# Performance work log

Measured on AMD Instinct MI355X. Metric: run time of the kernel, lower is better.

The kernel has to match this reference:

```python
import jax, jax.numpy as jnp
import numpy as np

N_Q = 4  # qubits = input_size
H_GATE = jnp.array([[1.0, 1.0], [1.0, -1.0]], dtype=jnp.complex64) / np.sqrt(2.0)
# efficient-kan grid: grid_size=1, spline_order=3, range [-1,1], h=2
KAN_GRID = np.arange(-3, 5, dtype=np.float32) * 2.0 - 1.0  # [-7,-5,-3,-1,1,3,5,7]
SPLINE_ORDER = 3


def nqe_embed(x):
    # [B, n] -> [B, 2n-1]: append (pi - x_i)(pi - x_{i+1}) ZZ-feature-map terms
    return jnp.concatenate([x, (jnp.pi - x[:, :-1]) * (jnp.pi - x[:, 1:])], axis=1)


def apply_1q(state, U, q):
    # state [B,2,2,2,2]; single-qubit gate U [2,2] on qubit q
    state = jnp.moveaxis(state, q + 1, -1)
    state = state @ U.T
    return jnp.moveaxis(state, -1, q + 1)


def apply_rz_batched(state, theta, q):
    # RZ(theta_b) with per-batch angles; diagonal gate -> elementwise phase
    ph = jnp.exp(-0.5j * theta)  # [B]
    diag = jnp.stack([ph, jnp.conj(ph)], axis=-1)  # [B,2]
    shape = [state.shape[0], 1, 1, 1, 1]
    shape[q + 1] = 2
    return state * diag.reshape(shape)


def apply_cnot(state, c, t):
    s = jnp.moveaxis(state, (c + 1, t + 1), (-2, -1))
    s = jnp.stack([s[..., 0, :], s[..., 1, ::-1]], axis=-2)
    return jnp.moveaxis(s, (-2, -1), (c + 1, t + 1))


def feature_map(state, angles):
    # IQP-style embedding: H on all, RZ(a_q), then ZZ(a_{n+i}) on neighbors (2n-1 angles)
    for q in range(N_Q):
        state = apply_1q(state, H_GATE, q)
    for q in range(N_Q):
        state = apply_rz_batched(state, angles[:, q], q)
    for i in range(N_Q - 1):
        state = apply_cnot(state, i, i + 1)
        state = apply_rz_batched(state, angles[:, N_Q + i], i + 1)
        state = apply_cnot(state, i, i + 1)
    return state


def rot_mat(phi, theta, omega):
    # pennylane Rot = RZ(omega) RY(theta) RZ(phi)
    c = jnp.cos(theta / 2).astype(jnp.complex64)
    s = jnp.sin(theta / 2).astype(jnp.complex64)
    a = jnp.exp(-0.5j * (phi + omega)) * c
    b = -jnp.exp(0.5j * (phi - omega)) * s
    d = jnp.exp(-0.5j * (phi - omega)) * s
    e = jnp.exp(0.5j * (phi + omega)) * c
    return jnp.stack([jnp.stack([a, b]), jnp.stack([d, e])])


def ansatz(state, params):
    # StronglyEntanglingLayers: 2 layers x (Rot per qubit + CNOT ring), params [24]
    p = params.reshape(2, N_Q, 3)
    for l in range(2):
        for q in range(N_Q):
            state = apply_1q(state, rot_mat(p[l, q, 0], p[l, q, 1], p[l, q, 2]), q)
        for q in range(N_Q):
            state = apply_cnot(state, q, (q + 1) % N_Q)
    return state


def quantum_cell(hidden_ang, input_ang, p1, p2):
    # one QRNN step: embed hidden, ansatz1, embed input, ansatz2, measure <Z_q>
    B = hidden_ang.shape[0]
    state = jnp.zeros((B, 2, 2, 2, 2), jnp.complex64).at[:, 0, 0, 0, 0].set(1.0)
    state = ansatz(feature_map(state, hidden_ang), p1)
    state = ansatz(feature_map(state, input_ang), p2)
    probs = jnp.abs(state) ** 2  # [B,2,2,2,2]
    sign = jnp.array([1.0, -1.0], jnp.float32)
    evs = []
    for q in range(N_Q):
        shape = [1, 1, 1, 1, 1]
        shape[q + 1] = 2
        evs.append(jnp.sum(probs * sign.reshape(shape), axis=(1, 2, 3, 4)))
    return jnp.stack(evs, axis=1)  # [B,4]


def kan_forward(x, base_w, spline_w):
    # efficient-kan KANLinear: silu base path + B-spline path (grid_size=1, order=3)
    grid = jnp.asarray(KAN_GRID)
    xg = x[..., None]  # [B,in,1]
    bases = ((xg >= grid[:-1]) & (xg < grid[1:])).astype(x.dtype)  # [B,in,7]
    for k in range(1, SPLINE_ORDER + 1):
        bases = ((xg - grid[: -(k + 1)]) / (grid[k:-1] - grid[: -(k + 1)]) * bases[..., :-1]
                 + (grid[k + 1:] - xg) / (grid[k + 1:] - grid[1:-k]) * bases[..., 1:])
    B = x.shape[0]
    base = jax.nn.silu(x) @ base_w.T
    spline = bases.reshape(B, -1) @ spline_w.reshape(spline_w.shape[0], -1).T
    return base + spline  # [B, 2n-1]


def setup_inputs() -> dict:
    key = jax.random.key(0)
    ks = jax.random.split(key, 10)
    B, S, n = 16384, 256, 4
    return {
        "inputs": jax.random.uniform(ks[0], (B, S, n), jnp.float32),
        "initial_t": jax.random.uniform(ks[1], (B, 2 * n - 1), jnp.float32),
        "ansatz_params_1": jax.random.uniform(ks[2], (24,), jnp.float32),
        "ansatz_params_2": jax.random.uniform(ks[3], (24,), jnp.float32),
        "kan_base_w": jax.random.normal(ks[4], (2 * n - 1, n), jnp.float32) * 0.1,
        "kan_spline_w": jax.random.normal(ks[5], (2 * n - 1, n, 4), jnp.float32) * 0.1,
        "cls_w1": jax.random.normal(ks[6], (16, n), jnp.float32) * 0.3,
        "cls_b1": jnp.zeros((16,), jnp.float32),
        "cls_w2": jax.random.normal(ks[7], (1, 16), jnp.float32) * 0.2,
        "cls_b2": jnp.zeros((1,), jnp.float32),
    }


def reference(inputs, initial_t, ansatz_params_1, ansatz_params_2, kan_base_w,
              kan_spline_w, cls_w1, cls_b1, cls_w2, cls_b2):
    # inputs [B,S,n]
    x0 = nqe_embed(inputs[:, 0])
    hidden = quantum_cell(initial_t, x0, ansatz_params_1, ansatz_params_2)  # [B,4]

    @jax.checkpoint
    def step(hidden, x_t):
        h_ang = kan_forward(hidden, kan_base_w, kan_spline_w)  # [B,7]
        x_emb = nqe_embed(x_t)  # [B,7]
        hidden = quantum_cell(h_ang, x_emb, ansatz_params_1, ansatz_params_2)
        return hidden, None

    xs = jnp.swapaxes(inputs[:, 1:], 0, 1)  # [S-1,B,n]
    hidden, _ = jax.lax.scan(step, hidden, xs)
    h = jax.nn.relu(hidden @ cls_w1.T + cls_b1)
    return h @ cls_w2.T + cls_b2  # [B,1]
```

## Files before the change

kernel.cpp:

```cpp
#include <hip/hip_runtime.h>
#include <math.h>

#define DEV static __device__ __forceinline__

typedef float v2 __attribute__((ext_vector_type(2)));

template<int CTRL>
DEV float qperm(float x) {
    return __int_as_float(__builtin_amdgcn_mov_dpp(__float_as_int(x), CTRL, 0xF, 0xF, true));
}
DEV float lx1(float v)  { return qperm<0xB1>(v); }
DEV float lx2(float v)  { return qperm<0x4E>(v); }
DEV float x3f_(float v) { return qperm<0x1B>(v); }
DEV float ror8(float v) { return qperm<0x128>(v); }
DEV float rfl(float x)  { return __int_as_float(__builtin_amdgcn_readfirstlane(__float_as_int(x))); }

DEV v2 ror8v(v2 a){ return (v2){ror8(a.x), ror8(a.y)}; }
DEV v2 lx1v(v2 a) { return (v2){lx1(a.x), lx1(a.y)}; }
DEV v2 lx2v(v2 a) { return (v2){lx2(a.x), lx2(a.y)}; }
DEV v2 x3v(v2 a)  { return (v2){x3f_(a.x), x3f_(a.y)}; }
DEV v2 r8lx1v(v2 a){ return (v2){ror8(lx1(a.x)), ror8(lx1(a.y))}; }
DEV v2 r8lx2v(v2 a){ return (v2){ror8(lx2(a.x)), ror8(lx2(a.y))}; }

DEV v2 vswap(v2 a)  { return __builtin_shufflevector(a, a, 1, 0); }
DEV v2 vsplat(float f) { return (v2){f, f}; }
DEV v2 vfma(v2 a, v2 b, v2 c) { return __builtin_elementwise_fma(a, b, c); }

DEV v2 gup(v2 A, v2 P, float dr, v2 di, float orr, v2 oi) {
    v2 n = A * dr;
    n = vfma(vswap(A), di, n);
    n = vfma(P, vsplat(orr), n);
    n = vfma(vswap(P), oi, n);
    return n;
}

DEV void fsincos(float rev, float* s, float* c) {
    float f = __builtin_amdgcn_fractf(rev);
    *s = __builtin_amdgcn_sinf(f);
    *c = __builtin_amdgcn_cosf(f);
}

__global__ __launch_bounds__(256, 2)
void qrnn_kernel(const float* __restrict__ inputs, const float* __restrict__ initial_t,
                 const float* __restrict__ p1, const float* __restrict__ p2,
                 const float* __restrict__ kbw, const float* __restrict__ ksw,
                 const float* __restrict__ w1, const float* __restrict__ cb1,
                 const float* __restrict__ w2, const float* __restrict__ cb2,
                 float* __restrict__ out, int B, int S)
{
    const int tid    = blockIdx.x * blockDim.x + threadIdx.x;
    const int lane16 = threadIdx.x & 15;
    const int e      = (tid >> 4) * 2 + ((lane16 >> 2) & 1);
    if (e >= B) return;
    const int sub    = lane16 & 3;
    const bool b1    = ((lane16 >> 3) & 1) != 0;
    const bool b2 = (sub & 1) != 0, b3 = (sub & 2) != 0;
    const float z2f = b2 ? -1.f : 1.f;
    const float z3f = b3 ? -1.f : 1.f;
    const float z1f = b1 ? -1.f : 1.f;
    const float z12 = z1f * z2f, z23 = z2f * z3f, z13 = z1f * z3f;
    const float z123 = z1f * z23;
    const bool is0 = (sub == 0), is1 = (sub == 1), is2 = (sub == 2);

    const float REVC = -0.07957747154594767f;

    float u00r[4][4], u00i[4][4], u01r[4][4], u01i[4][4];
    const float* PP[2] = { p1, p2 };
#pragma unroll
    for (int aI = 0; aI < 2; ++aI) {
        const float* pp = PP[aI];
#pragma unroll
        for (int l = 0; l < 2; ++l) {
            const int idx = aI*2 + l;
#pragma unroll
            for (int q = 0; q < 4; ++q) {
                float phi = pp[l*12 + q*3 + 0];
                float tht = pp[l*12 + q*3 + 1];
                float omg = pp[l*12 + q*3 + 2];
                float st, ct; sincosf(0.5f*tht, &st, &ct);
                float sA, cA, sB, cB;
                sincosf(0.5f*(phi + omg), &sA, &cA);
                sincosf(0.5f*(phi - omg), &sB, &cB);
                u00r[idx][q] = rfl( cA*ct); u00i[idx][q] = rfl(-sA*ct);
                u01r[idx][q] = rfl(-cB*st); u01i[idx][q] = rfl(-sB*st);
            }
        }
    }

    const float Sr0 = u00r[0][0], Tr0 = u01r[0][0];
    const v2 Sin0 = (v2){-u00i[0][0], u00i[0][0]};
    const v2 Tin0 = (v2){-u01i[0][0], u01i[0][0]};
    float U0r[3], B0r[3]; v2 A0n[3], W0n[3];
    {
        const float zq3[3] = { z1f, z2f, z3f };
#pragma unroll
        for (int q = 1; q < 4; ++q) {
            float z = zq3[q-1];
            U0r[q-1] = u00r[0][q];
            A0n[q-1] = (v2){-z*u00i[0][q], z*u00i[0][q]};
            B0r[q-1] = z*u01r[0][q];
            W0n[q-1] = (v2){-u01i[0][q], u01i[0][q]};
        }
    }
    float d1r[4], o1r[4]; v2 d1i[4], o1i[4];
    {
        const float zf1[4] = { z123, z1f, z12, z123 };
#pragma unroll
        for (int q = 0; q < 4; ++q) {
            float ar = u00r[1][q] - u01r[1][q];
            float ai = u00i[1][q] + u01i[1][q];
            float br = u00r[1][q] + u01r[1][q];
            float bi = u01i[1][q] - u00i[1][q];
            float z = zf1[q];
            d1r[q] = z*ar;
            d1i[q] = (v2){-ai, ai};
            o1r[q] = br;
            o1i[q] = (v2){-z*bi, z*bi};
        }
    }
    float s2r[4], t2r[4]; v2 s2i[4], t2i[4];
    {
        const float zf2[4] = { z23, z2f, z3f, z1f };
#pragma unroll
        for (int q = 0; q < 4; ++q) {
            float z = zf2[q];
            s2r[q] = u00r[2][q];
            s2i[q] = (v2){-z*u00i[2][q], z*u00i[2][q]};
            t2r[q] = z*u01r[2][q];
            t2i[q] = (v2){-u01i[2][q], u01i[2][q]};
        }
    }
    float s3r[4], t3r[4]; v2 s3i[4], t3i[4];
    {
        const float zf3[4] = { z123, z3f, 1.0f, z1f };
#pragma unroll
        for (int q = 0; q < 4; ++q) {
            float z = zf3[q];
            s3r[q] = u00r[3][q];
            s3i[q] = (v2){-z*u00i[3][q], z*u00i[3][q]};
            t3r[q] = z*u01r[3][q];
            t3i[q] = (v2){-u01i[3][q], u01i[3][q]};
        }
    }

    float kQ0[7], kQ1[7], kQ2[7], kQ3[7], kBW[7];
#pragma unroll
    for (int r = 0; r < 7; ++r) {
        float sw0 = ksw[r*16 + sub*4 + 0], sw1 = ksw[r*16 + sub*4 + 1];
        float sw2 = ksw[r*16 + sub*4 + 2], sw3 = ksw[r*16 + sub*4 + 3];
        const float f = REVC / 48.0f;
        kQ0[r] = f * (sw0 + 23.f*sw1 + 23.f*sw2 + sw3);
        kQ1[r] = f * (-3.f*sw0 - 15.f*sw1 + 15.f*sw2 + 3.f*sw3);
        kQ2[r] = f * (3.f*sw0 - 3.f*sw1 - 3.f*sw2 + 3.f*sw3);
        kQ3[r] = f * (-sw0 + 3.f*sw1 - 3.f*sw2 + sw3);
        kBW[r] = REVC * kbw[r*4 + sub];
    }
    const int pr0[3] = {0, 1, 3}, pr1[3] = {4, 2, 6};
    v2 Q0p[3], Q1p[3], Q2p[3], Q3p[3], BWp[3];
#pragma unroll
    for (int j = 0; j < 3; ++j) {
        Q0p[j] = (v2){kQ0[pr0[j]], kQ0[pr1[j]]};
        Q1p[j] = (v2){kQ1[pr0[j]], kQ1[pr1[j]]};
        Q2p[j] = (v2){kQ2[pr0[j]], kQ2[pr1[j]]};
        Q3p[j] = (v2){kQ3[pr0[j]], kQ3[pr1[j]]};
        BWp[j] = (v2){kBW[pr0[j]], kBW[pr1[j]]};
    }

    const float SCL = (is0 ? z13 : (is1 ? z12 : (is2 ? z12 : z2f))) * (1.0f/256.0f);

    v2 H04, H12, H36;
    float H5;
    const float4* inp4 = (const float4*)inputs;
    H04 = (v2){REVC*initial_t[e*7+0], REVC*initial_t[e*7+4]};
    H12 = (v2){REVC*initial_t[e*7+1], REVC*initial_t[e*7+2]};
    H36 = (v2){REVC*initial_t[e*7+3], REVC*initial_t[e*7+6]};
    H5  = REVC*initial_t[e*7+5];
    const long BASE = (long)e * S;
    float4 XC = inp4[BASE];

    const float NQPI = -0.7853981633974483f;
    float XK = 0.f;
    v2 A0, A1;

#pragma unroll 1
    for (int t = 0; t < S; ++t) {
        const int tn = (t + 1 < S) ? t + 1 : S - 1;
        float4 XN = inp4[BASE + tn];

        {
            float base = H12.x * z1f;
            base = fmaf(H12.y, z2f, base);
            base = fmaf(H36.x, z3f, base);
            base = fmaf(H5,   z12, base);
            base = fmaf(H36.y, z23, base);
            float w = fmaf(H04.y, z1f, H04.x);
            float s0, c0, s1, c1;
            fsincos(base + w, &s0, &c0);
            fsincos(base - w, &s1, &c1);
            A0 = (v2){c0, s0};
            A1 = (v2){c1, s1};
        }

        {
            v2 n0 = gup(A0, A1, Sr0,  Sin0,  Tr0, Tin0);
            v2 n1 = gup(A1, A0, Sr0, -Sin0, -Tr0, Tin0);
            A0 = n0; A1 = n1;
        }
        A0 = gup(A0, ror8v(A0), U0r[0], A0n[0], B0r[0], W0n[0]);
        A1 = gup(A1, ror8v(A1), U0r[0], A0n[0], B0r[0], W0n[0]);
        A0 = gup(A0, lx1v(A0), U0r[1], A0n[1], B0r[1], W0n[1]);
        A1 = gup(A1, lx1v(A1), U0r[1], A0n[1], B0r[1], W0n[1]);
        A0 = gup(A0, lx2v(A0), U0r[2], A0n[2], B0r[2], W0n[2]);
        A1 = gup(A1, lx2v(A1), U0r[2], A0n[2], B0r[2], W0n[2]);

        {
            v2 p0 = ror8v(A1), p1 = ror8v(A0);
            v2 n0 = gup(A0, p0, d1r[0], d1i[0], o1r[0], o1i[0]);
            v2 n1 = gup(A1, p1, d1r[0], d1i[0], o1r[0], o1i[0]);
            A0 = n0; A1 = n1;
        }
        A0 = gup(A0, r8lx1v(A0),  d1r[1], d1i[1], o1r[1],  o1i[1]);
        A1 = gup(A1, r8lx1v(A1), -d1r[1], d1i[1], o1r[1], -o1i[1]);
        A0 = gup(A0, x3v(A0),  d1r[2], d1i[2], o1r[2],  o1i[2]);
        A1 = gup(A1, x3v(A1), -d1r[2], d1i[2], o1r[2], -o1i[2]);
        {
            v2 p0 = r8lx2v(A1), p1 = r8lx2v(A0);
            v2 n0 = gup(A0, p0,  d1r[3], d1i[3], o1r[3],  o1i[3]);
            v2 n1 = gup(A1, p1, -d1r[3], d1i[3], o1r[3], -o1i[3]);
            A0 = n0; A1 = n1;
        }

        {
            float hx0 = REVC*XC.x, hx1 = REVC*XC.y;
            float hx2 = REVC*XC.z, hx3 = REVC*XC.w;
            float u0 = fmaf(4.f, hx0, 1.f);
            float u1 = fmaf(4.f, hx1, 1.f);
            float u2 = fmaf(4.f, hx2, 1.f);
            float u3 = fmaf(4.f, hx3, 1.f);
            float he4 = NQPI * (u0*u1);
            float he5 = NQPI * (u1*u2);
            float he6 = NQPI * (u2*u3);

            float base = hx1 * z2f;
            base = fmaf(hx2, z3f, base);
            base = fmaf(hx3, z1f, base);
            base = fmaf(he5, z23, base);
            base = fmaf(he6, z13, base);
            float w = fmaf(he4, z3f, hx0 * z23);
            float s0, c0, s1, c1;
            fsincos(base + w, &s0, &c0);
            fsincos(base - w, &s1, &c1);
            v2 sn0 = (v2){-s0, s0};
            v2 sn1 = (v2){-s1, s1};
            A0 = vfma(vswap(A0), sn0, A0 * c0);
            A1 = vfma(vswap(A1), sn1, A1 * c1);
        }

        {
            v2 n0 = gup(A0, A1, s2r[0],  s2i[0],  t2r[0], t2i[0]);
            v2 n1 = gup(A1, A0, s2r[0], -s2i[0], -t2r[0], t2i[0]);
            A0 = n0; A1 = n1;
        }
        {
            v2 p0 = lx1v(A1), p1 = lx1v(A0);
            v2 n0 = gup(A0, p0, s2r[1], s2i[1], t2r[1], t2i[1]);
            v2 n1 = gup(A1, p1, s2r[1], s2i[1], t2r[1], t2i[1]);
            A0 = n0; A1 = n1;
        }
        {
            v2 p0 = lx2v(A1), p1 = lx2v(A0);
            v2 n0 = gup(A0, p0, s2r[2], s2i[2], t2r[2], t2i[2]);
            v2 n1 = gup(A1, p1, s2r[2], s2i[2], t2r[2], t2i[2]);
            A0 = n0; A1 = n1;
        }
        A0 = gup(A0, ror8v(A0), s2r[3], s2i[3], t2r[3], t2i[3]);
        A1 = gup(A1, ror8v(A1), s2r[3], s2i[3], t2r[3], t2i[3]);

        A0 = gup(A0, lx1v(A0), s3r[0], s3i[0], t3r[0], t3i[0]);
        A1 = gup(A1, lx1v(A1), s3r[0], s3i[0], t3r[0], t3i[0]);
        A0 = gup(A0, x3v(A0),  s3r[1],  s3i[1],  t3r[1], t3i[1]);
        A1 = gup(A1, x3v(A1),  s3r[1], -s3i[1], -t3r[1], t3i[1]);
        {
            v2 p0 = r8lx2v(A1), p1 = r8lx2v(A0);
            v2 n0 = gup(A0, p0, s3r[2],  s3i[2],  t3r[2], t3i[2]);
            v2 n1 = gup(A1, p1, s3r[2], -s3i[2], -t3r[2], t3i[2]);
            A0 = n0; A1 = n1;
        }
        A0 = gup(A0, r8lx1v(A0), s3r[3],  s3i[3],  t3r[3], t3i[3]);
        A1 = gup(A1, r8lx1v(A1), s3r[3], -s3i[3], -t3r[3], t3i[3]);

        {
            v2 m0 = A0 * A0, m1 = A1 * A1;
            float pa = m0.x + m0.y;
            float pb = m1.x + m1.y;
            float s  = pa + pb;
            float dl = pa - pb;
            float rd = ror8(dl);
            float tA = dl - rd;
            float vA = dl + rd;
            float t1 = tA - lx1(tA); t1 += lx2(t1);
            float t0 = tA + lx1(tA); t0 -= lx2(t0);
            float v1 = vA - lx1(vA); v1 += lx2(v1);
            float wA = s - ror8(s);
            float w1m = wA - lx1(wA); w1m += lx2(w1m);
            float pre = is0 ? t0 : (is1 ? t1 : (is2 ? w1m : v1));
            XK = pre * SCL;
        }

        {
            float xk = XK;
            float eneg = __builtin_amdgcn_exp2f(xk * -1.44269504088896f);
            float silu = xk * __builtin_amdgcn_rcpf(1.0f + eneg);
            v2 xs = vsplat(xk), ss = vsplat(silu);
            v2 op[3];
#pragma unroll
            for (int k = 0; k < 3; ++k) {
                v2 o = vfma(Q3p[k], xs, Q2p[k]);
                o = vfma(o, xs, Q1p[k]);
                o = vfma(o, xs, Q0p[k]);
                o = vfma(BWp[k], ss, o);
                o = o + (v2){lx1(o.x), lx1(o.y)};
                o = o + (v2){lx2(o.x), lx2(o.y)};
                op[k] = o;
            }
            {
                float o = fmaf(kQ3[5], xk, kQ2[5]);
                o = fmaf(o, xk, kQ1[5]);
                o = fmaf(o, xk, kQ0[5]);
                o = fmaf(kBW[5], silu, o);
                o += lx1(o); o += lx2(o);
                H5 = o;
            }
            H04 = op[0]; H12 = op[1]; H36 = op[2];
            XC = XN;
        }
    }

    {
        float xk  = XK;
        float ev1 = qperm<0x55>(xk);
        float ev2 = qperm<0xAA>(xk);
        float ev3 = qperm<0xFF>(xk);
        if (sub == 0 && !b1) {
            float acc = cb2[0];
#pragma unroll
            for (int i = 0; i < 16; ++i) {
                float h = cb1[i] + w1[i*4+0]*xk + w1[i*4+1]*ev1
                        + w1[i*4+2]*ev2 + w1[i*4+3]*ev3;
                h = fmaxf(h, 0.0f);
                acc += w2[i]*h;
            }
            out[e] = acc;
        }
    }
}

extern "C" void kernel_launch(void* const* d_in, const int* in_sizes, int n_in,
                              void* d_out, int out_size, void* d_ws, size_t ws_size,
                              hipStream_t stream) {
    const float* inputs    = (const float*)d_in[0];
    const float* initial_t = (const float*)d_in[1];
    const float* p1        = (const float*)d_in[2];
    const float* p2        = (const float*)d_in[3];
    const float* kbw       = (const float*)d_in[4];
    const float* ksw       = (const float*)d_in[5];
    const float* w1        = (const float*)d_in[6];
    const float* cb1       = (const float*)d_in[7];
    const float* w2        = (const float*)d_in[8];
    const float* cb2       = (const float*)d_in[9];

    const int B = in_sizes[1] / 7;
    const int S = in_sizes[0] / (B * 4);

    const int threads = B * 8;
    const int block = 256;
    const int grid = (threads + block - 1) / block;

    qrnn_kernel<<<grid, block, 0, stream>>>(inputs, initial_t, p1, p2, kbw, ksw,
                                            w1, cb1, w2, cb2, (float*)d_out, B, S);
}
```

Measured before the change: 317.7 us.

## Map each batch element to four lanes holding four amplitudes each

Changes the thread-to-state mapping from eight lanes per batch element (two amplitudes each) to four lanes per element (four amplitudes each). Gates on qubit 1 that used cross-row DPP ror8 permutes now mix registers inside a lane, and launch bounds drop to one block per SIMD pair so more registers are available. This halves the thread count and removes row-rotate permutes. In exchange each lane does twice the arithmetic and holds more registers, so there are fewer waves to hide latency.

```diff
diff --git a/kernel.cpp b/kernel.cpp
--- a/kernel.cpp
+++ b/kernel.cpp
@@ -12,25 +12,22 @@
 DEV float lx1(float v)  { return qperm<0xB1>(v); }
 DEV float lx2(float v)  { return qperm<0x4E>(v); }
 DEV float x3f_(float v) { return qperm<0x1B>(v); }
-DEV float ror8(float v) { return qperm<0x128>(v); }
 DEV float rfl(float x)  { return __int_as_float(__builtin_amdgcn_readfirstlane(__float_as_int(x))); }
 
-DEV v2 ror8v(v2 a){ return (v2){ror8(a.x), ror8(a.y)}; }
 DEV v2 lx1v(v2 a) { return (v2){lx1(a.x), lx1(a.y)}; }
 DEV v2 lx2v(v2 a) { return (v2){lx2(a.x), lx2(a.y)}; }
 DEV v2 x3v(v2 a)  { return (v2){x3f_(a.x), x3f_(a.y)}; }
-DEV v2 r8lx1v(v2 a){ return (v2){ror8(lx1(a.x)), ror8(lx1(a.y))}; }
-DEV v2 r8lx2v(v2 a){ return (v2){ror8(lx2(a.x)), ror8(lx2(a.y))}; }
-
-DEV v2 vswap(v2 a)  { return __builtin_shufflevector(a, a, 1, 0); }
-DEV v2 vsplat(float f) { return (v2){f, f}; }
-DEV v2 vfma(v2 a, v2 b, v2 c) { return __builtin_elementwise_fma(a, b, c); }
-
-DEV v2 gup(v2 A, v2 P, float dr, v2 di, float orr, v2 oi) {
-    v2 n = A * dr;
-    n = vfma(vswap(A), di, n);
-    n = vfma(P, vsplat(orr), n);
-    n = vfma(vswap(P), oi, n);
+
+DEV v2 gup_s(v2 A, v2 P, float dr, float di, float orr, float oi) {
+    v2 n;
+    n.x = A.x*dr; n.x = fmaf(A.y, -di, n.x); n.x = fmaf(P.x, orr, n.x); n.x = fmaf(P.y, -oi, n.x);
+    n.y = A.y*dr; n.y = fmaf(A.x,  di, n.y); n.y = fmaf(P.y, orr, n.y); n.y = fmaf(P.x,  oi, n.y);
+    return n;
+}
+DEV v2 prot(v2 A, float c, float s) {
+    v2 n;
+    n.x = A.x*c; n.x = fmaf(A.y, -s, n.x);
+    n.y = A.y*c; n.y = fmaf(A.x,  s, n.y);
     return n;
 }
 
@@ -40,7 +37,7 @@
     *c = __builtin_amdgcn_cosf(f);
 }
 
-__global__ __launch_bounds__(256, 2)
+__global__ __launch_bounds__(256, 1)
 void qrnn_kernel(const float* __restrict__ inputs, const float* __restrict__ initial_t,
                  const float* __restrict__ p1, const float* __restrict__ p2,
                  const float* __restrict__ kbw, const float* __restrict__ ksw,
@@ -48,21 +45,18 @@
                  const float* __restrict__ w2, const float* __restrict__ cb2,
                  float* __restrict__ out, int B, int S)
 {
-    const int tid    = blockIdx.x * blockDim.x + threadIdx.x;
-    const int lane16 = threadIdx.x & 15;
-    const int e      = (tid >> 4) * 2 + ((lane16 >> 2) & 1);
+    const int tid = blockIdx.x * blockDim.x + threadIdx.x;
+    const int e   = tid >> 2;
     if (e >= B) return;
-    const int sub    = lane16 & 3;
-    const bool b1    = ((lane16 >> 3) & 1) != 0;
+    const int sub = threadIdx.x & 3;
     const bool b2 = (sub & 1) != 0, b3 = (sub & 2) != 0;
     const float z2f = b2 ? -1.f : 1.f;
     const float z3f = b3 ? -1.f : 1.f;
-    const float z1f = b1 ? -1.f : 1.f;
-    const float z12 = z1f * z2f, z23 = z2f * z3f, z13 = z1f * z3f;
-    const float z123 = z1f * z23;
+    const float z23 = z2f * z3f;
     const bool is0 = (sub == 0), is1 = (sub == 1), is2 = (sub == 2);
 
     const float REVC = -0.07957747154594767f;
+    const float NQPI = -0.7853981633974483f;
 
     float u00r[4][4], u00i[4][4], u01r[4][4], u01i[4][4];
     const float* PP[2] = { p1, p2 };
@@ -87,59 +81,43 @@
         }
     }
 
-    const float Sr0 = u00r[0][0], Tr0 = u01r[0][0];
-    const v2 Sin0 = (v2){-u00i[0][0], u00i[0][0]};
-    const v2 Tin0 = (v2){-u01i[0][0], u01i[0][0]};
-    float U0r[3], B0r[3]; v2 A0n[3], W0n[3];
+    float cdr[16], cdi[16], cor_[16], coi[16];
     {
-        const float zq3[3] = { z1f, z2f, z3f };
-#pragma unroll
-        for (int q = 1; q < 4; ++q) {
-            float z = zq3[q-1];
-            U0r[q-1] = u00r[0][q];
-            A0n[q-1] = (v2){-z*u00i[0][q], z*u00i[0][q]};
-            B0r[q-1] = z*u01r[0][q];
-            W0n[q-1] = (v2){-u01i[0][q], u01i[0][q]};
-        }
-    }
-    float d1r[4], o1r[4]; v2 d1i[4], o1i[4];
-    {
-        const float zf1[4] = { z123, z1f, z12, z123 };
+        const float f0[4] = {1.f, 1.f, z2f, z3f};
+#pragma unroll
+        for (int q = 0; q < 4; ++q) {
+            cdr[q]  = u00r[0][q];
+            cdi[q]  = f0[q]*u00i[0][q];
+            cor_[q] = f0[q]*u01r[0][q];
+            coi[q]  = u01i[0][q];
+        }
+        const float f1a[4] = {z23, 1.f, z2f, z23};
 #pragma unroll
         for (int q = 0; q < 4; ++q) {
             float ar = u00r[1][q] - u01r[1][q];
             float ai = u00i[1][q] + u01i[1][q];
             float br = u00r[1][q] + u01r[1][q];
             float bi = u01i[1][q] - u00i[1][q];
-            float z = zf1[q];
-            d1r[q] = z*ar;
-            d1i[q] = (v2){-ai, ai};
-            o1r[q] = br;
-            o1i[q] = (v2){-z*bi, z*bi};
-        }
-    }
-    float s2r[4], t2r[4]; v2 s2i[4], t2i[4];
-    {
-        const float zf2[4] = { z23, z2f, z3f, z1f };
+            cdr[4+q]  = f1a[q]*ar;
+            cdi[4+q]  = ai;
+            cor_[4+q] = br;
+            coi[4+q]  = f1a[q]*bi;
+        }
+        const float f2a[4] = {z23, z2f, z3f, 1.f};
 #pragma unroll
         for (int q = 0; q < 4; ++q) {
-            float z = zf2[q];
-            s2r[q] = u00r[2][q];
-            s2i[q] = (v2){-z*u00i[2][q], z*u00i[2][q]};
-            t2r[q] = z*u01r[2][q];
-            t2i[q] = (v2){-u01i[2][q], u01i[2][q]};
-        }
-    }
-    float s3r[4], t3r[4]; v2 s3i[4], t3i[4];
-    {
-        const float zf3[4] = { z123, z3f, 1.0f, z1f };
+            cdr[8+q]  = u00r[2][q];
+            cdi[8+q]  = f2a[q]*u00i[2][q];
+            cor_[8+q] = f2a[q]*u01r[2][q];
+            coi[8+q]  = u01i[2][q];
+        }
+        const float f3a[4] = {z23, z3f, 1.f, 1.f};
 #pragma unroll
         for (int q = 0; q < 4; ++q) {
-            float z = zf3[q];
-            s3r[q] = u00r[3][q];
-            s3i[q] = (v2){-z*u00i[3][q], z*u00i[3][q]};
-            t3r[q] = z*u01r[3][q];
-            t3i[q] = (v2){-u01i[3][q], u01i[3][q]};
+            cdr[12+q]  = u00r[3][q];
+            cdi[12+q]  = f3a[q]*u00i[3][q];
+            cor_[12+q] = f3a[q]*u01r[3][q];
+            coi[12+q]  = u01i[3][q];
         }
     }
 
@@ -166,7 +144,9 @@
         BWp[j] = (v2){kBW[pr0[j]], kBW[pr1[j]]};
     }
 
-    const float SCL = (is0 ? z13 : (is1 ? z12 : (is2 ? z12 : z2f))) * (1.0f/256.0f);
+    const float SCL = (is0 ? z3f : z2f) * (1.0f/256.0f);
+    const float zNQ3  = z3f * NQPI;
+    const float zNQ23 = z23 * NQPI;
 
     v2 H04, H12, H36;
     float H5;
@@ -178,9 +158,8 @@
     const long BASE = (long)e * S;
     float4 XC = inp4[BASE];
 
-    const float NQPI = -0.7853981633974483f;
     float XK = 0.f;
-    v2 A0, A1;
+    v2 a00, a01, a10, a11;
 
 #pragma unroll 1
     for (int t = 0; t < S; ++t) {
@@ -188,46 +167,71 @@
         float4 XN = inp4[BASE + tn];
 
         {
-            float base = H12.x * z1f;
-            base = fmaf(H12.y, z2f, base);
-            base = fmaf(H36.x, z3f, base);
-            base = fmaf(H5,   z12, base);
-            base = fmaf(H36.y, z23, base);
-            float w = fmaf(H04.y, z1f, H04.x);
-            float s0, c0, s1, c1;
-            fsincos(base + w, &s0, &c0);
-            fsincos(base - w, &s1, &c1);
-            A0 = (v2){c0, s0};
-            A1 = (v2){c1, s1};
-        }
-
-        {
-            v2 n0 = gup(A0, A1, Sr0,  Sin0,  Tr0, Tin0);
-            v2 n1 = gup(A1, A0, Sr0, -Sin0, -Tr0, Tin0);
-            A0 = n0; A1 = n1;
-        }
-        A0 = gup(A0, ror8v(A0), U0r[0], A0n[0], B0r[0], W0n[0]);
-        A1 = gup(A1, ror8v(A1), U0r[0], A0n[0], B0r[0], W0n[0]);
-        A0 = gup(A0, lx1v(A0), U0r[1], A0n[1], B0r[1], W0n[1]);
-        A1 = gup(A1, lx1v(A1), U0r[1], A0n[1], B0r[1], W0n[1]);
-        A0 = gup(A0, lx2v(A0), U0r[2], A0n[2], B0r[2], W0n[2]);
-        A1 = gup(A1, lx2v(A1), U0r[2], A0n[2], B0r[2], W0n[2]);
-
-        {
-            v2 p0 = ror8v(A1), p1 = ror8v(A0);
-            v2 n0 = gup(A0, p0, d1r[0], d1i[0], o1r[0], o1i[0]);
-            v2 n1 = gup(A1, p1, d1r[0], d1i[0], o1r[0], o1i[0]);
-            A0 = n0; A1 = n1;
-        }
-        A0 = gup(A0, r8lx1v(A0),  d1r[1], d1i[1], o1r[1],  o1i[1]);
-        A1 = gup(A1, r8lx1v(A1), -d1r[1], d1i[1], o1r[1], -o1i[1]);
-        A0 = gup(A0, x3v(A0),  d1r[2], d1i[2], o1r[2],  o1i[2]);
-        A1 = gup(A1, x3v(A1), -d1r[2], d1i[2], o1r[2], -o1i[2]);
-        {
-            v2 p0 = r8lx2v(A1), p1 = r8lx2v(A0);
-            v2 n0 = gup(A0, p0,  d1r[3], d1i[3], o1r[3],  o1i[3]);
-            v2 n1 = gup(A1, p1, -d1r[3], d1i[3], o1r[3], -o1i[3]);
-            A0 = n0; A1 = n1;
+            float c_ = z2f*H12.y;
+            c_ = fmaf(z3f, H36.x, c_);
+            c_ = fmaf(z23, H36.y, c_);
+            float d_ = fmaf(z2f, H5, H12.x);
+            float w0 = H04.x, w1 = H04.y;
+            float pd = c_ + d_, qd = c_ - d_;
+            float rw = w0 + w1, sw = w0 - w1;
+            float s00,c00,s01,c01,s10,c10,s11,c11;
+            fsincos(pd + rw, &s00, &c00);
+            fsincos(qd + sw, &s01, &c01);
+            fsincos(pd - rw, &s10, &c10);
+            fsincos(qd - sw, &s11, &c11);
+            a00 = (v2){c00, s00}; a01 = (v2){c01, s01};
+            a10 = (v2){c10, s10}; a11 = (v2){c11, s11};
+        }
+
+        {
+            v2 n00 = gup_s(a00, a10, cdr[0],  cdi[0],  cor_[0], coi[0]);
+            v2 n10 = gup_s(a10, a00, cdr[0], -cdi[0], -cor_[0], coi[0]);
+            v2 n01 = gup_s(a01, a11, cdr[0],  cdi[0],  cor_[0], coi[0]);
+            v2 n11 = gup_s(a11, a01, cdr[0], -cdi[0], -cor_[0], coi[0]);
+            a00=n00; a10=n10; a01=n01; a11=n11;
+        }
+        {
+            v2 n00 = gup_s(a00, a01, cdr[1],  cdi[1],  cor_[1], coi[1]);
+            v2 n01 = gup_s(a01, a00, cdr[1], -cdi[1], -cor_[1], coi[1]);
+            v2 n10 = gup_s(a10, a11, cdr[1],  cdi[1],  cor_[1], coi[1]);
+            v2 n11 = gup_s(a11, a10, cdr[1], -cdi[1], -cor_[1], coi[1]);
+            a00=n00; a01=n01; a10=n10; a11=n11;
+        }
+        a00 = gup_s(a00, lx1v(a00), cdr[2], cdi[2], cor_[2], coi[2]);
+        a01 = gup_s(a01, lx1v(a01), cdr[2], cdi[2], cor_[2], coi[2]);
+        a10 = gup_s(a10, lx1v(a10), cdr[2], cdi[2], cor_[2], coi[2]);
+        a11 = gup_s(a11, lx1v(a11), cdr[2], cdi[2], cor_[2], coi[2]);
+        a00 = gup_s(a00, lx2v(a00), cdr[3], cdi[3], cor_[3], coi[3]);
+        a01 = gup_s(a01, lx2v(a01), cdr[3], cdi[3], cor_[3], coi[3]);
+        a10 = gup_s(a10, lx2v(a10), cdr[3], cdi[3], cor_[3], coi[3]);
+        a11 = gup_s(a11, lx2v(a11), cdr[3], cdi[3], cor_[3], coi[3]);
+
+        {
+            v2 n00 = gup_s(a00, a11,  cdr[4], cdi[4], cor_[4],  coi[4]);
+            v2 n01 = gup_s(a01, a10, -cdr[4], cdi[4], cor_[4], -coi[4]);
+            v2 n10 = gup_s(a10, a01,  cdr[4], cdi[4], cor_[4],  coi[4]);
+            v2 n11 = gup_s(a11, a00, -cdr[4], cdi[4], cor_[4], -coi[4]);
+            a00=n00; a01=n01; a10=n10; a11=n11;
+        }
+        {
+            v2 p00 = lx1v(a01), p01 = lx1v(a00), p10 = lx1v(a11), p11 = lx1v(a10);
+            v2 n00 = gup_s(a00, p00,  cdr[5], cdi[5], cor_[5],  coi[5]);
+            v2 n01 = gup_s(a01, p01, -cdr[5], cdi[5], cor_[5], -coi[5]);
+            v2 n10 = gup_s(a10, p10, -cdr[5], cdi[5], cor_[5], -coi[5]);
+            v2 n11 = gup_s(a11, p11,  cdr[5], cdi[5], cor_[5],  coi[5]);
+            a00=n00; a01=n01; a10=n10; a11=n11;
+        }
+        a00 = gup_s(a00, x3v(a00),  cdr[6], cdi[6], cor_[6],  coi[6]);
+        a01 = gup_s(a01, x3v(a01), -cdr[6], cdi[6], cor_[6], -coi[6]);
+        a10 = gup_s(a10, x3v(a10), -cdr[6], cdi[6], cor_[6], -coi[6]);
+        a11 = gup_s(a11, x3v(a11),  cdr[6], cdi[6], cor_[6],  coi[6]);
+        {
+            v2 p00 = lx2v(a11), p01 = lx2v(a10), p10 = lx2v(a01), p11 = lx2v(a00);
+            v2 n00 = gup_s(a00, p00,  cdr[7], cdi[7], cor_[7],  coi[7]);
+            v2 n01 = gup_s(a01, p01, -cdr[7], cdi[7], cor_[7], -coi[7]);
+            v2 n10 = gup_s(a10, p10, -cdr[7], cdi[7], cor_[7], -coi[7]);
+            v2 n11 = gup_s(a11, p11,  cdr[7], cdi[7], cor_[7],  coi[7]);
+            a00=n00; a01=n01; a10=n10; a11=n11;
         }
 
         {
@@ -237,73 +241,99 @@
             float u1 = fmaf(4.f, hx1, 1.f);
             float u2 = fmaf(4.f, hx2, 1.f);
             float u3 = fmaf(4.f, hx3, 1.f);
-            float he4 = NQPI * (u0*u1);
-            float he5 = NQPI * (u1*u2);
-            float he6 = NQPI * (u2*u3);
-
-            float base = hx1 * z2f;
-            base = fmaf(hx2, z3f, base);
-            base = fmaf(hx3, z1f, base);
-            base = fmaf(he5, z23, base);
-            base = fmaf(he6, z13, base);
-            float w = fmaf(he4, z3f, hx0 * z23);
-            float s0, c0, s1, c1;
-            fsincos(base + w, &s0, &c0);
-            fsincos(base - w, &s1, &c1);
-            v2 sn0 = (v2){-s0, s0};
-            v2 sn1 = (v2){-s1, s1};
-            A0 = vfma(vswap(A0), sn0, A0 * c0);
-            A1 = vfma(vswap(A1), sn1, A1 * c1);
-        }
-
-        {
-            v2 n0 = gup(A0, A1, s2r[0],  s2i[0],  t2r[0], t2i[0]);
-            v2 n1 = gup(A1, A0, s2r[0], -s2i[0], -t2r[0], t2i[0]);
-            A0 = n0; A1 = n1;
-        }
-        {
-            v2 p0 = lx1v(A1), p1 = lx1v(A0);
-            v2 n0 = gup(A0, p0, s2r[1], s2i[1], t2r[1], t2i[1]);
-            v2 n1 = gup(A1, p1, s2r[1], s2i[1], t2r[1], t2i[1]);
-            A0 = n0; A1 = n1;
-        }
-        {
-            v2 p0 = lx2v(A1), p1 = lx2v(A0);
-            v2 n0 = gup(A0, p0, s2r[2], s2i[2], t2r[2], t2i[2]);
-            v2 n1 = gup(A1, p1, s2r[2], s2i[2], t2r[2], t2i[2]);
-            A0 = n0; A1 = n1;
-        }
-        A0 = gup(A0, ror8v(A0), s2r[3], s2i[3], t2r[3], t2i[3]);
-        A1 = gup(A1, ror8v(A1), s2r[3], s2i[3], t2r[3], t2i[3]);
-
-        A0 = gup(A0, lx1v(A0), s3r[0], s3i[0], t3r[0], t3i[0]);
-        A1 = gup(A1, lx1v(A1), s3r[0], s3i[0], t3r[0], t3i[0]);
-        A0 = gup(A0, x3v(A0),  s3r[1],  s3i[1],  t3r[1], t3i[1]);
-        A1 = gup(A1, x3v(A1),  s3r[1], -s3i[1], -t3r[1], t3i[1]);
-        {
-            v2 p0 = r8lx2v(A1), p1 = r8lx2v(A0);
-            v2 n0 = gup(A0, p0, s3r[2],  s3i[2],  t3r[2], t3i[2]);
-            v2 n1 = gup(A1, p1, s3r[2], -s3i[2], -t3r[2], t3i[2]);
-            A0 = n0; A1 = n1;
-        }
-        A0 = gup(A0, r8lx1v(A0), s3r[3],  s3i[3],  t3r[3], t3i[3]);
-        A1 = gup(A1, r8lx1v(A1), s3r[3], -s3i[3], -t3r[3], t3i[3]);
-
-        {
-            v2 m0 = A0 * A0, m1 = A1 * A1;
-            float pa = m0.x + m0.y;
-            float pb = m1.x + m1.y;
-            float s  = pa + pb;
-            float dl = pa - pb;
-            float rd = ror8(dl);
-            float tA = dl - rd;
-            float vA = dl + rd;
-            float t1 = tA - lx1(tA); t1 += lx2(t1);
-            float t0 = tA + lx1(tA); t0 -= lx2(t0);
-            float v1 = vA - lx1(vA); v1 += lx2(v1);
-            float wA = s - ror8(s);
-            float w1m = wA - lx1(wA); w1m += lx2(w1m);
-            float pre = is0 ? t0 : (is1 ? t1 : (is2 ? w1m : v1));
+            float h4r = u0*u1, h5r = u1*u2, h6r = u2*u3;
+            float c2 = z2f*hx1;
+            c2 = fmaf(z3f, hx2, c2);
+            c2 = fmaf(zNQ23, h5r, c2);
+            float d2 = fmaf(zNQ3, h6r, hx3);
+            float w2 = fmaf(zNQ3, h4r, z23*hx0);
+            float p2 = c2 + d2, q2v = c2 - d2;
+            float s00,c00,s01,c01,s10,c10,s11,c11;
+            fsincos(p2 + w2,  &s00, &c00);
+            fsincos(q2v + w2, &s01, &c01);
+            fsincos(p2 - w2,  &s10, &c10);
+            fsincos(q2v - w2, &s11, &c11);
+            a00 = prot(a00, c00, s00);
+            a01 = prot(a01, c01, s01);
+            a10 = prot(a10, c10, s10);
+            a11 = prot(a11, c11, s11);
+        }
+
+        {
+            v2 n00 = gup_s(a00, a10, cdr[8],  cdi[8],  cor_[8], coi[8]);
+            v2 n10 = gup_s(a10, a00, cdr[8], -cdi[8], -cor_[8], coi[8]);
+            v2 n01 = gup_s(a01, a11, cdr[8],  cdi[8],  cor_[8], coi[8]);
+            v2 n11 = gup_s(a11, a01, cdr[8], -cdi[8], -cor_[8], coi[8]);
+            a00=n00; a10=n10; a01=n01; a11=n11;
+        }
+        {
+            v2 p00 = lx1v(a10), p10 = lx1v(a00), p01 = lx1v(a11), p11 = lx1v(a01);
+            v2 n00 = gup_s(a00, p00, cdr[9], cdi[9], cor_[9], coi[9]);
+            v2 n10 = gup_s(a10, p10, cdr[9], cdi[9], cor_[9], coi[9]);
+            v2 n01 = gup_s(a01, p01, cdr[9], cdi[9], cor_[9], coi[9]);
+            v2 n11 = gup_s(a11, p11, cdr[9], cdi[9], cor_[9], coi[9]);
+            a00=n00; a10=n10; a01=n01; a11=n11;
+        }
+        {
+            v2 p00 = lx2v(a10), p10 = lx2v(a00), p01 = lx2v(a11), p11 = lx2v(a01);
+            v2 n00 = gup_s(a00, p00, cdr[10], cdi[10], cor_[10], coi[10]);
+            v2 n10 = gup_s(a10, p10, cdr[10], cdi[10], cor_[10], coi[10]);
+            v2 n01 = gup_s(a01, p01, cdr[10], cdi[10], cor_[10], coi[10]);
+            v2 n11 = gup_s(a11, p11, cdr[10], cdi[10], cor_[10], coi[10]);
+            a00=n00; a10=n10; a01=n01; a11=n11;
+        }
+        {
+            v2 n00 = gup_s(a00, a01, cdr[11],  cdi[11],  cor_[11], coi[11]);
+            v2 n01 = gup_s(a01, a00, cdr[11], -cdi[11], -cor_[11], coi[11]);
+            v2 n10 = gup_s(a10, a11, cdr[11],  cdi[11],  cor_[11], coi[11]);
+            v2 n11 = gup_s(a11, a10, cdr[11], -cdi[11], -cor_[11], coi[11]);
+            a00=n00; a01=n01; a10=n10; a11=n11;
+        }
+
+        a00 = gup_s(a00, lx1v(a00), cdr[12],  cdi[12],  cor_[12], coi[12]);
+        a01 = gup_s(a01, lx1v(a01), cdr[12], -cdi[12], -cor_[12], coi[12]);
+        a10 = gup_s(a10, lx1v(a10), cdr[12],  cdi[12],  cor_[12], coi[12]);
+        a11 = gup_s(a11, lx1v(a11), cdr[12], -cdi[12], -cor_[12], coi[12]);
+        a00 = gup_s(a00, x3v(a00), cdr[13],  cdi[13],  cor_[13], coi[13]);
+        a01 = gup_s(a01, x3v(a01), cdr[13],  cdi[13],  cor_[13], coi[13]);
+        a10 = gup_s(a10, x3v(a10), cdr[13], -cdi[13], -cor_[13], coi[13]);
+        a11 = gup_s(a11, x3v(a11), cdr[13], -cdi[13], -cor_[13], coi[13]);
+        {
+            v2 p00 = lx2v(a11), p01 = lx2v(a10), p10 = lx2v(a01), p11 = lx2v(a00);
+            v2 n00 = gup_s(a00, p00, cdr[14],  cdi[14],  cor_[14], coi[14]);
+            v2 n01 = gup_s(a01, p01, cdr[14],  cdi[14],  cor_[14], coi[14]);
+            v2 n10 = gup_s(a10, p10, cdr[14], -cdi[14], -cor_[14], coi[14]);
+            v2 n11 = gup_s(a11, p11, cdr[14], -cdi[14], -cor_[14], coi[14]);
+            a00=n00; a01=n01; a10=n10; a11=n11;
+        }
+        {
+            v2 p00 = lx1v(a01), p01 = lx1v(a00), p10 = lx1v(a11), p11 = lx1v(a10);
+            v2 n00 = gup_s(a00, p00, cdr[15],  cdi[15],  cor_[15], coi[15]);
+            v2 n01 = gup_s(a01, p01, cdr[15], -cdi[15], -cor_[15], coi[15]);
+            v2 n10 = gup_s(a10, p10, cdr[15], -cdi[15], -cor_[15], coi[15]);
+            v2 n11 = gup_s(a11, p11, cdr[15],  cdi[15],  cor_[15], coi[15]);
+            a00=n00; a01=n01; a10=n10; a11=n11;
+        }
+
+        {
+            float m00 = fmaf(a00.y, a00.y, a00.x*a00.x);
+            float m01 = fmaf(a01.y, a01.y, a01.x*a01.x);
+            float m10 = fmaf(a10.y, a10.y, a10.x*a10.x);
+            float m11 = fmaf(a11.y, a11.y, a11.x*a11.x);
+            float g_ = m00 - m01, h_ = m10 - m11;
+            float dl01 = g_ - h_;
+            float sn1  = g_ + h_;
+            float dn0  = (m00 + m01) - (m10 + m11);
+            float l1a = lx1(dl01);
+            float up = dl01 + l1a;
+            float um = dl01 - l1a;
+            float t0 = up - lx2(up);
+            float t1 = um + lx2(um);
+            float vm = sn1 - lx1(sn1);
+            float t2 = vm + lx2(vm);
+            float wm = dn0 - lx1(dn0);
+            float t3 = wm + lx2(wm);
+            float pre = is0 ? t0 : (is1 ? t1 : (is2 ? t2 : t3));
             XK = pre * SCL;
         }
 
@@ -311,14 +341,14 @@
             float xk = XK;
             float eneg = __builtin_amdgcn_exp2f(xk * -1.44269504088896f);
             float silu = xk * __builtin_amdgcn_rcpf(1.0f + eneg);
-            v2 xs = vsplat(xk), ss = vsplat(silu);
+            v2 xs = (v2){xk, xk}, ss = (v2){silu, silu};
             v2 op[3];
 #pragma unroll
             for (int k = 0; k < 3; ++k) {
-                v2 o = vfma(Q3p[k], xs, Q2p[k]);
-                o = vfma(o, xs, Q1p[k]);
-                o = vfma(o, xs, Q0p[k]);
-                o = vfma(BWp[k], ss, o);
+                v2 o = __builtin_elementwise_fma(Q3p[k], xs, Q2p[k]);
+                o = __builtin_elementwise_fma(o, xs, Q1p[k]);
+                o = __builtin_elementwise_fma(o, xs, Q0p[k]);
+                o = __builtin_elementwise_fma(BWp[k], ss, o);
                 o = o + (v2){lx1(o.x), lx1(o.y)};
                 o = o + (v2){lx2(o.x), lx2(o.y)};
                 op[k] = o;
@@ -341,7 +371,7 @@
         float ev1 = qperm<0x55>(xk);
         float ev2 = qperm<0xAA>(xk);
         float ev3 = qperm<0xFF>(xk);
-        if (sub == 0 && !b1) {
+        if (is0) {
             float acc = cb2[0];
 #pragma unroll
             for (int i = 0; i < 16; ++i) {
@@ -372,7 +402,7 @@
     const int B = in_sizes[1] / 7;
     const int S = in_sizes[0] / (B * 4);
 
-    const int threads = B * 8;
+    const int threads = B * 4;
     const int block = 256;
     const int grid = (threads + block - 1) / block;
 
```

New measurement: 282.1 us. 11.2% less time.
